# Optimization experiments

Measured on AMD Instinct MI355X. Metric: run time of the kernel, lower is better.

Reference implementation:

```python
import jax, jax.numpy as jnp
import numpy as np

N = 50000      # nodes
E = 200000     # edges
F_IN = 128     # input features
H = 1024       # hidden
C = 16         # classes
K = 3          # TAGConv hops
EPS = 1e-5


def setup_inputs() -> dict:
    key = jax.random.key(0)
    ks = jax.random.split(key, 12)
    s = 0.02
    x = jax.random.normal(ks[0], (N, F_IN), jnp.float32)
    edge_index = jax.random.randint(ks[1], (2, E), 0, N, dtype=jnp.int64)
    weight = jax.random.uniform(ks[2], (E,), jnp.float32)
    return {
        "x": x,
        "edge_index": edge_index,
        "weight": weight,
        "W1": jax.random.normal(ks[3], (K + 1, F_IN, H), jnp.float32) * s,
        "b1": jnp.zeros((H,), jnp.float32),
        "g1": jnp.ones((H,), jnp.float32),
        "be1": jnp.zeros((H,), jnp.float32),
        "a1": jnp.ones((H,), jnp.float32),
        "W2": jax.random.normal(ks[4], (K + 1, H, H), jnp.float32) * s,
        "b2": jnp.zeros((H,), jnp.float32),
        "g2": jnp.ones((H,), jnp.float32),
        "be2": jnp.zeros((H,), jnp.float32),
        "a2": jnp.ones((H,), jnp.float32),
        "W3": jax.random.normal(ks[5], (K + 1, H, C), jnp.float32) * s,
        "b3": jnp.zeros((C,), jnp.float32),
    }


def _edge_norm(weight, src, dst):
    # gcn_norm without self-loops: deg from edge weights at target nodes
    deg = jax.ops.segment_sum(weight, dst, num_segments=N)
    safe = jnp.where(deg > 0, deg, 1.0)
    dinv = jnp.where(deg > 0, jax.lax.rsqrt(safe), 0.0)
    norm_w = dinv[src] * weight * dinv[dst]
    cnt = jax.ops.segment_sum(jnp.ones((E,), weight.dtype), dst, num_segments=N)
    cnt_inv = jnp.where(cnt > 0, 1.0 / jnp.where(cnt > 0, cnt, 1.0), 0.0)
    return norm_w, cnt_inv


def _tagconv(x, W, b, src, dst, norm_w, cnt_inv):
    # out = sum_k lin_k(x_k), x_k = mean-aggr of norm_w * x_{k-1}[src] at dst
    out = x @ W[0]
    h = x
    for k in range(1, K + 1):
        msg = norm_w[:, None] * h[src]                       # [E, d]
        h = jax.ops.segment_sum(msg, dst, num_segments=N) * cnt_inv[:, None]
        out = out + h @ W[k]
    return out + b


def _graphnorm(x, g, be, a):
    # single graph: per-graph stats = global stats over nodes
    mean = jnp.mean(x, axis=0)
    out = x - a * mean
    var = jnp.mean(out * out, axis=0)
    return g * out / jnp.sqrt(var + EPS) + be


def reference(x, edge_index, weight, W1, b1, g1, be1, a1,
              W2, b2, g2, be2, a2, W3, b3):
    src, dst = edge_index[0], edge_index[1]
    norm_w, cnt_inv = _edge_norm(weight, src, dst)
    h = jax.nn.elu(_tagconv(x, W1, b1, src, dst, norm_w, cnt_inv))
    h = _graphnorm(h, g1, be1, a1)
    h = jax.nn.elu(_tagconv(h, W2, b2, src, dst, norm_w, cnt_inv))
    h = _graphnorm(h, g2, be2, a2)
    return _tagconv(h, W3, b3, src, dst, norm_w, cnt_inv)
```

## Files before the change

### kernel.cpp

```cpp
#include <hip/hip_runtime.h>
#include <hip/hip_bf16.h>
#include <math.h>

#define N_NODES 50000
#define N_EDGES 200000
#define FIN 128
#define HID 1024
#define NCLS 16
#define EPSN 1e-5f
#define NPAD 50048
#define MT 391
#define EPITCH 136

typedef __attribute__((ext_vector_type(8))) short short8;
typedef __attribute__((ext_vector_type(8))) unsigned short ushort8;
typedef __attribute__((ext_vector_type(4))) unsigned short u16x4;
typedef __attribute__((ext_vector_type(4))) float f32x4;

static __device__ __forceinline__ float bf2f(unsigned short u) {
  union { unsigned int i; float f; } v; v.i = ((unsigned int)u) << 16; return v.f;
}
static __device__ __forceinline__ unsigned short f2bf(float f) {
  __hip_bfloat16 h = __float2bfloat16(f);
  return *(unsigned short*)&h;
}

#define ASYNC16(gsrc, ldst)                                                   \
  __builtin_amdgcn_global_load_lds(                                           \
      (const __attribute__((address_space(1))) void*)(gsrc),                  \
      (__attribute__((address_space(3))) void*)(ldst), 16, 0, 0)


__global__ __launch_bounds__(256) void k_deg_cnt(const int* __restrict__ dst,
                                                 const float* __restrict__ w,
                                                 float* deg, int* cnt) {
  int e = blockIdx.x * 256 + threadIdx.x;
  if (e < N_EDGES) {
    int d = dst[e];
    atomicAdd(&deg[d], w[e]);
    atomicAdd(&cnt[d], 1);
  }
}

__global__ __launch_bounds__(256) void k_normw(const int* __restrict__ src,
                                               const int* __restrict__ dst,
                                               const float* __restrict__ w,
                                               const float* __restrict__ deg,
                                               float* __restrict__ normw) {
  int e = blockIdx.x * 256 + threadIdx.x;
  if (e < N_EDGES) {
    float ds = deg[src[e]], dd = deg[dst[e]];
    float a = ds > 0.f ? rsqrtf(ds) : 0.f;
    float b = dd > 0.f ? rsqrtf(dd) : 0.f;
    normw[e] = a * w[e] * b;
  }
}

__global__ __launch_bounds__(256) void k_cntinv(const int* __restrict__ cnt,
                                                float* __restrict__ cnt_inv) {
  int n = blockIdx.x * 256 + threadIdx.x;
  if (n < N_NODES) {
    int c = cnt[n];
    cnt_inv[n] = c > 0 ? 1.f / (float)c : 0.f;
  }
}

__global__ __launch_bounds__(1024) void k_scan_a(const int* __restrict__ cnt,
                                                 int* __restrict__ rowptr,
                                                 int* __restrict__ bsums) {
  __shared__ int sm[1024];
  int tid = threadIdx.x;
  int i = blockIdx.x * 1024 + tid;
  int v = (i < N_NODES) ? cnt[i] : 0;
  sm[tid] = v;
  __syncthreads();
  for (int off = 1; off < 1024; off <<= 1) {
    int t = (tid >= off) ? sm[tid - off] : 0;
    __syncthreads();
    sm[tid] += t;
    __syncthreads();
  }
  if (i < N_NODES) rowptr[i] = sm[tid] - v;
  if (tid == 1023) bsums[blockIdx.x] = sm[1023];
}

__global__ void k_scan_b(int* bsums, int nb) {
  if (threadIdx.x == 0 && blockIdx.x == 0) {
    int s = 0;
    for (int i = 0; i < nb; ++i) { int t = bsums[i]; bsums[i] = s; s += t; }
  }
}

__global__ __launch_bounds__(1024) void k_scan_c(int* __restrict__ rowptr,
                                                 const int* __restrict__ bsums) {
  int i = blockIdx.x * 1024 + threadIdx.x;
  if (i < N_NODES) rowptr[i] += bsums[blockIdx.x];
}

__global__ __launch_bounds__(256) void k_fill(const int* __restrict__ src,
                                              const int* __restrict__ dst,
                                              const float* __restrict__ normw,
                                              const int* __restrict__ rowptr,
                                              int* __restrict__ fill,
                                              int2* __restrict__ csr_ew) {
  int e = blockIdx.x * 256 + threadIdx.x;
  if (e < N_EDGES) {
    int d = dst[e];
    int pos = rowptr[d] + atomicAdd(&fill[d], 1);
    csr_ew[pos] = make_int2(src[e], __float_as_int(normw[e]));
  }
}


__global__ void k_transpose_bf16(const float* __restrict__ in,
                                 __hip_bfloat16* __restrict__ out, int K, int N) {
  __shared__ float tile[32][33];
  int kb = blockIdx.x * 32, nb = blockIdx.y * 32;
  int tx = threadIdx.x, ty = threadIdx.y;
  for (int i = ty; i < 32; i += 8) tile[i][tx] = in[(size_t)(kb + i) * N + nb + tx];
  __syncthreads();
  for (int i = ty; i < 32; i += 8)
    out[(size_t)(nb + i) * K + kb + tx] = __float2bfloat16(tile[tx][i]);
}

__global__ void k_transpose_scale_bf16(const float* __restrict__ in,
                                       __hip_bfloat16* __restrict__ out, int K, int N,
                                       const float* __restrict__ alpha) {
  __shared__ float tile[32][33];
  int kb = blockIdx.x * 32, nb = blockIdx.y * 32;
  int tx = threadIdx.x, ty = threadIdx.y;
  for (int i = ty; i < 32; i += 8) tile[i][tx] = in[(size_t)(kb + i) * N + nb + tx];
  __syncthreads();
  float sc = alpha[(kb + tx) & (HID - 1)];
  for (int i = ty; i < 32; i += 8)
    out[(size_t)(nb + i) * K + kb + tx] = __float2bfloat16(tile[tx][i] * sc);
}

__global__ __launch_bounds__(256) void k_ck_part(const float* __restrict__ W2,
                                                 const float* __restrict__ beta,
                                                 const float* __restrict__ b2,
                                                 float* __restrict__ ck) {
  int k3 = blockIdx.x;
  int ch = blockIdx.y;
  int tid = threadIdx.x;
  float acc[4] = {0.f, 0.f, 0.f, 0.f};
  const float* Wk = W2 + (size_t)k3 * HID * HID;
  int i0 = ch * 64;
  for (int in = i0; in < i0 + 64; ++in) {
    float s = beta[in];
    const float* row = Wk + (size_t)in * HID;
#pragma unroll
    for (int j = 0; j < 4; ++j) acc[j] += s * row[tid + j * 256];
  }
#pragma unroll
  for (int j = 0; j < 4; ++j) {
    float v = acc[j];
    if (k3 == 0 && ch == 0) v += b2[tid + j * 256];
    atomicAdd(&ck[k3 * HID + tid + j * 256], v);
  }
}

__global__ __launch_bounds__(64) void k_ck3(const float* __restrict__ W3,
                                            const float* __restrict__ beta,
                                            float* __restrict__ ck3) {
  int t = threadIdx.x;
  int k = t >> 4, j = t & 15;
  float acc = 0.f;
  for (int in = 0; in < HID; ++in)
    acc += beta[in] * W3[((size_t)k * HID + in) * 16 + j];
  ck3[t] = acc;
}

__global__ __launch_bounds__(256) void k_packw3(const float* __restrict__ W3,
                                                __hip_bfloat16* __restrict__ W3T,
                                                const float* __restrict__ alpha) {
  int idx = blockIdx.x * 256 + threadIdx.x;
  if (idx < 4 * 1024 * 16) {
    int k3 = idx >> 14, r = idx & 16383, k = r >> 4, j = r & 15;
    W3T[(size_t)(k3 * 16 + j) * 1024 + k] = __float2bfloat16(W3[idx] * alpha[k]);
  }
}

__global__ __launch_bounds__(256) void k_x_to_bf16(const float* __restrict__ x,
                                                   unsigned short* __restrict__ xc) {
  int i = blockIdx.x * 256 + threadIdx.x;
  if (i < N_NODES * FIN / 4) {
    int n = i >> 5, c4 = i & 31;
    const float4 v = ((const float4*)x)[i];
    u16x4 o;
    o[0] = f2bf(v.x); o[1] = f2bf(v.y); o[2] = f2bf(v.z); o[3] = f2bf(v.w);
    *(u16x4*)&xc[(size_t)n * 512 + c4 * 4] = o;
  }
}


template <int W>
__global__ __launch_bounds__(256) void k_spmm_v(
    const unsigned short* __restrict__ src_t, int sp,
    unsigned short* __restrict__ dst_t, int dp,
    const int* __restrict__ rowptr, const int* __restrict__ cnt,
    const float* __restrict__ cnt_inv,
    const int2* __restrict__ csr_ew) {
  constexpr int G = W / 8;
  int gl = blockIdx.x * 256 + threadIdx.x;
  int node = gl / G;
  if (node >= N_NODES) return;
  int fl = (gl % G) * 8;
  int beg = rowptr[node], end = beg + cnt[node];
  float acc[8] = {0.f, 0.f, 0.f, 0.f, 0.f, 0.f, 0.f, 0.f};
  int i = beg;
  for (; i + 1 < end; i += 2) {
    int2 e0 = csr_ew[i], e1 = csr_ew[i + 1];
    float w0 = __int_as_float(e0.y), w1 = __int_as_float(e1.y);
    ushort8 v0 = *(const ushort8*)&src_t[(size_t)e0.x * sp + fl];
    ushort8 v1 = *(const ushort8*)&src_t[(size_t)e1.x * sp + fl];
#pragma unroll
    for (int j = 0; j < 8; ++j) acc[j] += w0 * bf2f(v0[j]) + w1 * bf2f(v1[j]);
  }
  if (i < end) {
    int2 e0 = csr_ew[i];
    float w0 = __int_as_float(e0.y);
    ushort8 v0 = *(const ushort8*)&src_t[(size_t)e0.x * sp + fl];
#pragma unroll
    for (int j = 0; j < 8; ++j) acc[j] += w0 * bf2f(v0[j]);
  }
  float ci = cnt_inv[node];
  ushort8 o;
#pragma unroll
  for (int j = 0; j < 8; ++j) o[j] = f2bf(acc[j] * ci);
  *(ushort8*)&dst_t[(size_t)node * dp + fl] = o;
}

__global__ __launch_bounds__(256) void k_spmm16(const float* __restrict__ src_t, int sp,
                                                const float* __restrict__ addend, int ap,
                                                const float* __restrict__ b3,
                                                float* __restrict__ out, int op,
                                                const int* __restrict__ rowptr,
                                                const int* __restrict__ cnt,
                                                const float* __restrict__ cnt_inv,
                                                const int2* __restrict__ csr_ew) {
  int idx = blockIdx.x * 256 + threadIdx.x;
  if (idx >= N_NODES * 16) return;
  int node = idx >> 4, f = idx & 15;
  int beg = rowptr[node], ne = cnt[node];
  float acc = 0.f;
  for (int i = 0; i < ne; ++i) {
    int2 e = csr_ew[beg + i];
    acc += __int_as_float(e.y) * src_t[(size_t)e.x * sp + f];
  }
  float r = acc * cnt_inv[node] + addend[(size_t)node * ap + f];
  if (b3) r += b3[f];
  out[(size_t)node * op + f] = r;
}


__global__ __launch_bounds__(256, 4) void k_gemm(
    const unsigned short* __restrict__ A, int lda,
    const unsigned short* __restrict__ BT, int ldb,
    const unsigned short* __restrict__ Cinit, int ldci,
    void* __restrict__ Cout, int ldc, int cbf16,
    int M, int Nout, int K,
    const float* __restrict__ bias, int do_elu) {
  __shared__ __align__(16) unsigned short smem[128 * EPITCH];
  int tid = threadIdx.x;
  int wave = tid >> 6, lane = tid & 63;
  int wm = wave >> 1, wn = wave & 1;
  int l15 = lane & 15, quad = lane >> 4;
  int im = blockIdx.y, in_ = blockIdx.x;

  f32x4 acc[4][4];
  if (Cinit) {
    {
      int r = tid >> 1, hf = tid & 1;
      const unsigned short* gsrc =
          &Cinit[(size_t)(im * 128 + r) * ldci + in_ * 128 + hf * 64];
#pragma unroll
      for (int v = 0; v < 8; ++v)
        *(ushort8*)&smem[r * EPITCH + hf * 64 + v * 8] = *(const ushort8*)&gsrc[v * 8];
    }
    __syncthreads();
#pragma unroll
    for (int i = 0; i < 4; ++i)
#pragma unroll
      for (int j = 0; j < 4; ++j)
#pragma unroll
        for (int reg = 0; reg < 4; ++reg)
          acc[i][j][reg] =
              bf2f(smem[(wm * 64 + i * 16 + quad * 4 + reg) * EPITCH + wn * 64 + j * 16 + l15]);
    __syncthreads();
  } else {
#pragma unroll
    for (int i = 0; i < 4; ++i)
#pragma unroll
      for (int j = 0; j < 4; ++j) acc[i][j] = (f32x4){0.f, 0.f, 0.f, 0.f};
  }

  int srow = tid >> 2;
  int sl = (tid & 3) ^ (srow & 3) ^ ((srow >> 2) & 3);
  const unsigned short* gA0 = &A[(size_t)(im * 128 + srow) * lda + sl * 8];
  const unsigned short* gA1 = &A[(size_t)(im * 128 + 64 + srow) * lda + sl * 8];
  const unsigned short* gB0 = &BT[(size_t)(in_ * 128 + srow) * ldb + sl * 8];
  const unsigned short* gB1 = &BT[(size_t)(in_ * 128 + 64 + srow) * ldb + sl * 8];
  unsigned short* ldsA = smem;
  unsigned short* ldsB = smem + 8192;
  int woff0 = (wave * 64) * 8;
  int woff1 = (256 + wave * 64) * 8;
  int rsl = (quad ^ (l15 & 3) ^ (l15 >> 2)) * 8;

  auto stage = [&](int k0, int p) {
    ASYNC16(gA0 + k0, &ldsA[p * 4096 + woff0]);
    ASYNC16(gA1 + k0, &ldsA[p * 4096 + woff1]);
    ASYNC16(gB0 + k0, &ldsB[p * 4096 + woff0]);
    ASYNC16(gB1 + k0, &ldsB[p * 4096 + woff1]);
  };
  auto compute = [&](int p) {
    short8 af[4], bf[4];
#pragma unroll
    for (int i = 0; i < 4; ++i)
      af[i] = *(const short8*)&ldsA[p * 4096 + (wm * 64 + i * 16 + l15) * 32 + rsl];
#pragma unroll
    for (int j = 0; j < 4; ++j)
      bf[j] = *(const short8*)&ldsB[p * 4096 + (wn * 64 + j * 16 + l15) * 32 + rsl];
#pragma unroll
    for (int i = 0; i < 4; ++i)
#pragma unroll
      for (int j = 0; j < 4; ++j)
        acc[i][j] = __builtin_amdgcn_mfma_f32_16x16x32_bf16(af[i], bf[j], acc[i][j], 0, 0, 0);
  };

  stage(0, 0);
  __syncthreads();
  int p = 0;
  for (int k0 = 32; k0 < K; k0 += 32) {
    stage(k0, p ^ 1);
    compute(p);
    __syncthreads();
    p ^= 1;
  }
  compute(p);
  __syncthreads();

  if (cbf16) {
#pragma unroll
    for (int i = 0; i < 4; ++i)
#pragma unroll
      for (int j = 0; j < 4; ++j) {
        int cg = in_ * 128 + wn * 64 + j * 16 + l15;
        float bv = bias ? bias[cg] : 0.f;
#pragma unroll
        for (int reg = 0; reg < 4; ++reg) {
          float v = acc[i][j][reg] + bv;
          if (do_elu) v = v > 0.f ? v : expm1f(v);
          smem[(wm * 64 + i * 16 + quad * 4 + reg) * EPITCH + wn * 64 + j * 16 + l15] = f2bf(v);
        }
      }
    __syncthreads();
    int r = tid >> 1, hf = tid & 1;
    unsigned short* gdst =
        (unsigned short*)Cout + (size_t)(im * 128 + r) * ldc + in_ * 128 + hf * 64;
#pragma unroll
    for (int v = 0; v < 8; ++v)
      *(ushort8*)&gdst[v * 8] = *(const ushort8*)&smem[r * EPITCH + hf * 64 + v * 8];
  } else {
#pragma unroll
    for (int i = 0; i < 4; ++i) {
      int r0 = im * 128 + wm * 64 + i * 16 + quad * 4;
#pragma unroll
      for (int j = 0; j < 4; ++j) {
        int c = in_ * 128 + wn * 64 + j * 16 + l15;
        if (c < Nout) {
#pragma unroll
          for (int reg = 0; reg < 4; ++reg) {
            int r = r0 + reg;
            if (r < M) {
              float v = acc[i][j][reg];
              if (bias) v += bias[c];
              if (do_elu) v = v > 0.f ? v : expm1f(v);
              ((float*)Cout)[(size_t)r * ldc + c] = v;
            }
          }
        }
      }
    }
  }
}


__global__ __launch_bounds__(512) void k_colstats(const unsigned short* __restrict__ h,
                                                  float* __restrict__ stats) {
  __shared__ float sm[4 * 2048];
  int tid = threadIdx.x;
  int f0 = (tid & 127) * 8;
  int q = tid >> 7;
  int r0 = blockIdx.y * 128 + q * 32;
  int r1 = r0 + 32; if (r1 > N_NODES) r1 = N_NODES;
  float s[8] = {0,0,0,0,0,0,0,0}, s2[8] = {0,0,0,0,0,0,0,0};
  for (int r = r0; r < r1; ++r) {
    ushort8 v = *(const ushort8*)&h[(size_t)r * HID + f0];
#pragma unroll
    for (int j = 0; j < 8; ++j) { float x = bf2f(v[j]); s[j] += x; s2[j] += x * x; }
  }
#pragma unroll
  for (int j = 0; j < 8; ++j) {
    sm[q * 2048 + f0 + j] = s[j];
    sm[q * 2048 + 1024 + f0 + j] = s2[j];
  }
  __syncthreads();
  for (int idx = tid; idx < 2048; idx += 512) {
    float v = sm[idx] + sm[2048 + idx] + sm[4096 + idx] + sm[6144 + idx];
    atomicAdd(&stats[idx], v);
  }
}

__global__ __launch_bounds__(256) void k_finalize(const float* __restrict__ g,
                                                  const float* __restrict__ be,
                                                  const float* __restrict__ a,
                                                  float* __restrict__ stats) {
  int f = blockIdx.x * 256 + threadIdx.x;
  if (f < HID) {
    float m = stats[f] / (float)N_NODES;
    float ex2 = stats[HID + f] / (float)N_NODES;
    float av = a[f];
    float var = ex2 - 2.f * av * m * m + av * av * m * m;
    float alpha = g[f] * rsqrtf(var + EPSN);
    stats[2 * HID + f] = alpha;
    stats[3 * HID + f] = be[f] - alpha * av * m;
  }
}


extern "C" void kernel_launch(void* const* d_in, const int* in_sizes, int n_in,
                              void* d_out, int out_size, void* d_ws, size_t ws_size,
                              hipStream_t stream) {
  const float* x   = (const float*)d_in[0];
  const int*   ei  = (const int*)d_in[1];
  const float* w   = (const float*)d_in[2];
  const float* W1  = (const float*)d_in[3];
  const float* b1  = (const float*)d_in[4];
  const float* g1  = (const float*)d_in[5];
  const float* be1 = (const float*)d_in[6];
  const float* a1  = (const float*)d_in[7];
  const float* W2  = (const float*)d_in[8];
  const float* b2  = (const float*)d_in[9];
  const float* g2  = (const float*)d_in[10];
  const float* be2 = (const float*)d_in[11];
  const float* a2  = (const float*)d_in[12];
  const float* W3  = (const float*)d_in[13];
  const float* b3  = (const float*)d_in[14];
  float* out = (float*)d_out;

  const int* srcI = ei;
  const int* dstI = ei + N_EDGES;

  char* base = (char*)d_ws;
  size_t off = 0;
  auto alloc = [&](size_t bytes) -> char* {
    char* p = base + off;
    off += (bytes + 255) & ~(size_t)255;
    return p;
  };

  float* deg      = (float*)alloc(N_NODES * 4);
  int*   cnt      = (int*)alloc(N_NODES * 4);
  float* cnt_inv  = (float*)alloc(N_NODES * 4);
  float* normw    = (float*)alloc(N_EDGES * 4);
  int*   rowptr   = (int*)alloc((N_NODES + 1) * 4);
  int*   fill     = (int*)alloc(N_NODES * 4);
  int*   bsums    = (int*)alloc(64 * 4);
  int2*  csr_ew   = (int2*)alloc((size_t)N_EDGES * 8);
  float* stats    = (float*)alloc(4 * HID * 4);
  float* ck       = (float*)alloc(4 * HID * 4);
  float* ck3      = (float*)alloc(64 * 4);
  __hip_bfloat16* W1T = (__hip_bfloat16*)alloc((size_t)1024 * 512 * 2);
  __hip_bfloat16* W2T = (__hip_bfloat16*)alloc((size_t)1024 * 4096 * 2);
  __hip_bfloat16* W3T = (__hip_bfloat16*)alloc((size_t)128 * 1024 * 2);
  const size_t FT = (size_t)NPAD * HID * 2;
  unsigned short* T0 = (unsigned short*)alloc(FT);
  unsigned short* T1 = (unsigned short*)alloc(FT);
  size_t rem = (ws_size > off) ? (ws_size - off) : 0;
  bool full = rem >= FT + 1024;
  unsigned short *T2 = nullptr, *Q = nullptr, *R = nullptr;
  int wcols = 0;
  if (full) {
    T2 = (unsigned short*)alloc(FT);
  } else {
    wcols = 512;
    if (rem < 2 * (size_t)NPAD * 512 * 2 + 1024) wcols = 256;
    if (wcols == 256 && rem < 2 * (size_t)NPAD * 256 * 2 + 1024) wcols = 128;
    Q = (unsigned short*)alloc((size_t)NPAD * wcols * 2);
    R = (unsigned short*)alloc((size_t)NPAD * wcols * 2);
  }
  float* Z  = (float*)T0;
  float* t0 = (float*)((char*)T0 + (size_t)16 * 1024 * 1024);
  float* t1 = (float*)((char*)T0 + (size_t)24 * 1024 * 1024);
  (void)n_in; (void)in_sizes; (void)out_size;

  const int EB = (N_EDGES + 255) / 256;
  const int NB = (N_NODES + 255) / 256;

  (void)hipMemsetAsync(deg, 0, N_NODES * 4, stream);
  (void)hipMemsetAsync(cnt, 0, N_NODES * 4, stream);
  (void)hipMemsetAsync(fill, 0, N_NODES * 4, stream);
  k_deg_cnt<<<EB, 256, 0, stream>>>(dstI, w, deg, cnt);
  k_normw<<<EB, 256, 0, stream>>>(srcI, dstI, w, deg, normw);
  k_cntinv<<<NB, 256, 0, stream>>>(cnt, cnt_inv);
  k_scan_a<<<49, 1024, 0, stream>>>(cnt, rowptr, bsums);
  k_scan_b<<<1, 64, 0, stream>>>(bsums, 49);
  k_scan_c<<<49, 1024, 0, stream>>>(rowptr, bsums);
  k_fill<<<EB, 256, 0, stream>>>(srcI, dstI, normw, rowptr, fill, csr_ew);

  k_transpose_bf16<<<dim3(512 / 32, 1024 / 32), dim3(32, 8), 0, stream>>>(W1, W1T, 512, 1024);

  const unsigned short* W2Tu = (const unsigned short*)W2T;

  k_x_to_bf16<<<(N_NODES * FIN / 4 + 255) / 256, 256, 0, stream>>>(x, T1);
  {
    int blocks = (N_NODES * 16 + 255) / 256;
    for (int k = 1; k <= 3; ++k)
      k_spmm_v<128><<<blocks, 256, 0, stream>>>(
          T1 + (k - 1) * FIN, 512, T1 + k * FIN, 512,
          rowptr, cnt, cnt_inv, csr_ew);
  }
  k_gemm<<<dim3(8, MT), 256, 0, stream>>>(
      T1, 512, (const unsigned short*)W1T, 512,
      nullptr, 0, T0, HID, 1, N_NODES, HID, 512, b1, 1);
  (void)hipMemsetAsync(stats, 0, 2 * HID * 4, stream);
  k_colstats<<<dim3(1, MT), 512, 0, stream>>>(T0, stats);
  k_finalize<<<4, 256, 0, stream>>>(g1, be1, a1, stats);
  k_transpose_scale_bf16<<<dim3(4096 / 32, 1024 / 32), dim3(32, 8), 0, stream>>>(
      W2, W2T, 4096, 1024, stats + 2 * HID);
  (void)hipMemsetAsync(ck, 0, 4 * HID * 4, stream);
  k_ck_part<<<dim3(4, 16), 256, 0, stream>>>(W2, stats + 3 * HID, b2, ck);

  if (full) {
    const int SPB = (N_NODES * 128 + 255) / 256;
    k_gemm<<<dim3(8, MT), 256, 0, stream>>>(
        T0, 1024, W2Tu + 3 * 1024, 4096,
        nullptr, 0, T1, 1024, 1, N_NODES, 1024, 1024, ck + 3 * 1024, 0);
    k_spmm_v<1024><<<SPB, 256, 0, stream>>>(T1, 1024, T2, 1024,
                                            rowptr, cnt, cnt_inv, csr_ew);
    k_gemm<<<dim3(8, MT), 256, 0, stream>>>(
        T0, 1024, W2Tu + 2 * 1024, 4096,
        T2, 1024, T1, 1024, 1, N_NODES, 1024, 1024, ck + 2 * 1024, 0);
    k_spmm_v<1024><<<SPB, 256, 0, stream>>>(T1, 1024, T2, 1024,
                                            rowptr, cnt, cnt_inv, csr_ew);
    k_gemm<<<dim3(8, MT), 256, 0, stream>>>(
        T0, 1024, W2Tu + 1 * 1024, 4096,
        T2, 1024, T1, 1024, 1, N_NODES, 1024, 1024, ck + 1 * 1024, 0);
    k_spmm_v<1024><<<SPB, 256, 0, stream>>>(T1, 1024, T2, 1024,
                                            rowptr, cnt, cnt_inv, csr_ew);
    k_gemm<<<dim3(8, MT), 256, 0, stream>>>(
        T0, 1024, W2Tu + 0 * 1024, 4096,
        T2, 1024, T1, 1024, 1, N_NODES, 1024, 1024, ck + 0 * 1024, 1);
  } else {
    auto spmm_w = [&](const unsigned short* s, unsigned short* d) {
      int blocks = (N_NODES * (wcols / 8) + 255) / 256;
      if (wcols == 512)
        k_spmm_v<512><<<blocks, 256, 0, stream>>>(s, wcols, d, wcols,
            rowptr, cnt, cnt_inv, csr_ew);
      else if (wcols == 256)
        k_spmm_v<256><<<blocks, 256, 0, stream>>>(s, wcols, d, wcols,
            rowptr, cnt, cnt_inv, csr_ew);
      else
        k_spmm_v<128><<<blocks, 256, 0, stream>>>(s, wcols, d, wcols,
            rowptr, cnt, cnt_inv, csr_ew);
    };
    for (int c = 0; c < HID; c += wcols) {
      const unsigned short* Wb = W2Tu + (size_t)c * 4096;
      k_gemm<<<dim3(wcols / 128, MT), 256, 0, stream>>>(
          T0, 1024, Wb + 3 * 1024, 4096,
          nullptr, 0, Q, wcols, 1, N_NODES, wcols, 1024, ck + 3 * 1024 + c, 0);
      spmm_w(Q, R);
      k_gemm<<<dim3(wcols / 128, MT), 256, 0, stream>>>(
          T0, 1024, Wb + 2 * 1024, 4096,
          R, wcols, Q, wcols, 1, N_NODES, wcols, 1024, ck + 2 * 1024 + c, 0);
      spmm_w(Q, R);
      k_gemm<<<dim3(wcols / 128, MT), 256, 0, stream>>>(
          T0, 1024, Wb + 1 * 1024, 4096,
          R, wcols, Q, wcols, 1, N_NODES, wcols, 1024, ck + 1 * 1024 + c, 0);
      spmm_w(Q, R);
      k_gemm<<<dim3(wcols / 128, MT), 256, 0, stream>>>(
          T0, 1024, Wb + 0 * 1024, 4096,
          R, wcols, T1 + c, 1024, 1, N_NODES, wcols, 1024, ck + 0 * 1024 + c, 1);
    }
  }
  (void)hipMemsetAsync(stats, 0, 2 * HID * 4, stream);
  k_colstats<<<dim3(1, MT), 512, 0, stream>>>(T1, stats);
  k_finalize<<<4, 256, 0, stream>>>(g2, be2, a2, stats);
  k_packw3<<<(65536 + 255) / 256, 256, 0, stream>>>(W3, W3T, stats + 2 * HID);
  k_ck3<<<1, 64, 0, stream>>>(W3, stats + 3 * HID, ck3);

  k_gemm<<<dim3(1, MT), 256, 0, stream>>>(
      T1, 1024, (const unsigned short*)W3T, 1024,
      nullptr, 0, Z, 64, 0, N_NODES, 64, 1024, ck3, 0);
  const int SB = (N_NODES * 16 + 255) / 256;
  k_spmm16<<<SB, 256, 0, stream>>>(Z + 48, 64, Z + 32, 64, nullptr, t0, 16,
                                   rowptr, cnt, cnt_inv, csr_ew);
  k_spmm16<<<SB, 256, 0, stream>>>(t0, 16, Z + 16, 64, nullptr, t1, 16,
                                   rowptr, cnt, cnt_inv, csr_ew);
  k_spmm16<<<SB, 256, 0, stream>>>(t1, 16, Z + 0, 64, b3, out, 16,
                                   rowptr, cnt, cnt_inv, csr_ew);
}
```

Baseline: 1.835 ms.

## Fuse column statistics into GEMM epilogue, fold cnt_inv into edge weights, widen SpMM

Removes the separate column-statistics pass by accumulating per-column sum and sum-of-squares of the bf16 outputs inside the GEMM epilogue, reduced through shared memory and added with atomics. This avoids re-reading the full 50000x1024 activation twice. It also pre-multiplies the mean-aggregation factor cnt_inv into the CSR edge weights and merges the normw and cnt_inv kernels. The 1024-wide SpMM now handles 16 features per thread instead of 8. The costs are extra epilogue work and atomics in the GEMM, and fewer threads in the wide SpMM.

```diff
diff --git a/kernel.cpp b/kernel.cpp
--- a/kernel.cpp
+++ b/kernel.cpp
@@ -42,11 +42,13 @@
   }
 }
 
-__global__ __launch_bounds__(256) void k_normw(const int* __restrict__ src,
-                                               const int* __restrict__ dst,
-                                               const float* __restrict__ w,
-                                               const float* __restrict__ deg,
-                                               float* __restrict__ normw) {
+__global__ __launch_bounds__(256) void k_normw_cntinv(const int* __restrict__ src,
+                                                      const int* __restrict__ dst,
+                                                      const float* __restrict__ w,
+                                                      const float* __restrict__ deg,
+                                                      const int* __restrict__ cnt,
+                                                      float* __restrict__ normw,
+                                                      float* __restrict__ cnt_inv) {
   int e = blockIdx.x * 256 + threadIdx.x;
   if (e < N_EDGES) {
     float ds = deg[src[e]], dd = deg[dst[e]];
@@ -54,14 +56,9 @@
     float b = dd > 0.f ? rsqrtf(dd) : 0.f;
     normw[e] = a * w[e] * b;
   }
-}
-
-__global__ __launch_bounds__(256) void k_cntinv(const int* __restrict__ cnt,
-                                                float* __restrict__ cnt_inv) {
-  int n = blockIdx.x * 256 + threadIdx.x;
-  if (n < N_NODES) {
-    int c = cnt[n];
-    cnt_inv[n] = c > 0 ? 1.f / (float)c : 0.f;
+  if (e < N_NODES) {
+    int c = cnt[e];
+    cnt_inv[e] = c > 0 ? 1.f / (float)c : 0.f;
   }
 }
 
@@ -100,6 +97,7 @@
 __global__ __launch_bounds__(256) void k_fill(const int* __restrict__ src,
                                               const int* __restrict__ dst,
                                               const float* __restrict__ normw,
+                                              const float* __restrict__ cnt_inv,
                                               const int* __restrict__ rowptr,
                                               int* __restrict__ fill,
                                               int2* __restrict__ csr_ew) {
@@ -107,7 +105,7 @@
   if (e < N_EDGES) {
     int d = dst[e];
     int pos = rowptr[d] + atomicAdd(&fill[d], 1);
-    csr_ew[pos] = make_int2(src[e], __float_as_int(normw[e]));
+    csr_ew[pos] = make_int2(src[e], __float_as_int(normw[e] * cnt_inv[d]));
   }
 }
 
@@ -194,41 +192,55 @@
 }
 
 
-template <int W>
+template <int W, int FPL>
 __global__ __launch_bounds__(256) void k_spmm_v(
     const unsigned short* __restrict__ src_t, int sp,
     unsigned short* __restrict__ dst_t, int dp,
     const int* __restrict__ rowptr, const int* __restrict__ cnt,
-    const float* __restrict__ cnt_inv,
     const int2* __restrict__ csr_ew) {
-  constexpr int G = W / 8;
+  constexpr int G = W / FPL;
+  constexpr int NV = FPL / 8;
   int gl = blockIdx.x * 256 + threadIdx.x;
   int node = gl / G;
   if (node >= N_NODES) return;
-  int fl = (gl % G) * 8;
+  int fl = (gl % G) * FPL;
   int beg = rowptr[node], end = beg + cnt[node];
-  float acc[8] = {0.f, 0.f, 0.f, 0.f, 0.f, 0.f, 0.f, 0.f};
+  float acc[FPL];
+#pragma unroll
+  for (int j = 0; j < FPL; ++j) acc[j] = 0.f;
   int i = beg;
   for (; i + 1 < end; i += 2) {
     int2 e0 = csr_ew[i], e1 = csr_ew[i + 1];
     float w0 = __int_as_float(e0.y), w1 = __int_as_float(e1.y);
-    ushort8 v0 = *(const ushort8*)&src_t[(size_t)e0.x * sp + fl];
-    ushort8 v1 = *(const ushort8*)&src_t[(size_t)e1.x * sp + fl];
-#pragma unroll
-    for (int j = 0; j < 8; ++j) acc[j] += w0 * bf2f(v0[j]) + w1 * bf2f(v1[j]);
+    ushort8 v0[NV], v1[NV];
+#pragma unroll
+    for (int h = 0; h < NV; ++h) {
+      v0[h] = *(const ushort8*)&src_t[(size_t)e0.x * sp + fl + h * 8];
+      v1[h] = *(const ushort8*)&src_t[(size_t)e1.x * sp + fl + h * 8];
+    }
+#pragma unroll
+    for (int h = 0; h < NV; ++h)
+#pragma unroll
+      for (int j = 0; j < 8; ++j)
+        acc[h * 8 + j] += w0 * bf2f(v0[h][j]) + w1 * bf2f(v1[h][j]);
   }
   if (i < end) {
     int2 e0 = csr_ew[i];
     float w0 = __int_as_float(e0.y);
-    ushort8 v0 = *(const ushort8*)&src_t[(size_t)e0.x * sp + fl];
-#pragma unroll
-    for (int j = 0; j < 8; ++j) acc[j] += w0 * bf2f(v0[j]);
-  }
-  float ci = cnt_inv[node];
-  ushort8 o;
-#pragma unroll
-  for (int j = 0; j < 8; ++j) o[j] = f2bf(acc[j] * ci);
-  *(ushort8*)&dst_t[(size_t)node * dp + fl] = o;
+#pragma unroll
+    for (int h = 0; h < NV; ++h) {
+      ushort8 v0 = *(const ushort8*)&src_t[(size_t)e0.x * sp + fl + h * 8];
+#pragma unroll
+      for (int j = 0; j < 8; ++j) acc[h * 8 + j] += w0 * bf2f(v0[j]);
+    }
+  }
+#pragma unroll
+  for (int h = 0; h < NV; ++h) {
+    ushort8 o;
+#pragma unroll
+    for (int j = 0; j < 8; ++j) o[j] = f2bf(acc[h * 8 + j]);
+    *(ushort8*)&dst_t[(size_t)node * dp + fl + h * 8] = o;
+  }
 }
 
 __global__ __launch_bounds__(256) void k_spmm16(const float* __restrict__ src_t, int sp,
@@ -237,7 +249,6 @@
                                                 float* __restrict__ out, int op,
                                                 const int* __restrict__ rowptr,
                                                 const int* __restrict__ cnt,
-                                                const float* __restrict__ cnt_inv,
                                                 const int2* __restrict__ csr_ew) {
   int idx = blockIdx.x * 256 + threadIdx.x;
   if (idx >= N_NODES * 16) return;
@@ -248,7 +259,7 @@
     int2 e = csr_ew[beg + i];
     acc += __int_as_float(e.y) * src_t[(size_t)e.x * sp + f];
   }
-  float r = acc * cnt_inv[node] + addend[(size_t)node * ap + f];
+  float r = acc + addend[(size_t)node * ap + f];
   if (b3) r += b3[f];
   out[(size_t)node * op + f] = r;
 }
@@ -260,7 +271,8 @@
     const unsigned short* __restrict__ Cinit, int ldci,
     void* __restrict__ Cout, int ldc, int cbf16,
     int M, int Nout, int K,
-    const float* __restrict__ bias, int do_elu) {
+    const float* __restrict__ bias, int do_elu,
+    float* __restrict__ stats_out, int stats_off) {
   __shared__ __align__(16) unsigned short smem[128 * EPITCH];
   int tid = threadIdx.x;
   int wave = tid >> 6, lane = tid & 63;
@@ -341,6 +353,7 @@
   __syncthreads();
 
   if (cbf16) {
+    float sl0[4] = {0.f, 0.f, 0.f, 0.f}, sl2[4] = {0.f, 0.f, 0.f, 0.f};
 #pragma unroll
     for (int i = 0; i < 4; ++i)
 #pragma unroll
@@ -351,16 +364,48 @@
         for (int reg = 0; reg < 4; ++reg) {
           float v = acc[i][j][reg] + bv;
           if (do_elu) v = v > 0.f ? v : expm1f(v);
-          smem[(wm * 64 + i * 16 + quad * 4 + reg) * EPITCH + wn * 64 + j * 16 + l15] = f2bf(v);
+          unsigned short b = f2bf(v);
+          smem[(wm * 64 + i * 16 + quad * 4 + reg) * EPITCH + wn * 64 + j * 16 + l15] = b;
+          if (stats_out) {
+            int r = im * 128 + wm * 64 + i * 16 + quad * 4 + reg;
+            if (r < M) {
+              float vq = bf2f(b);
+              sl0[j] += vq; sl2[j] += vq * vq;
+            }
+          }
         }
       }
     __syncthreads();
-    int r = tid >> 1, hf = tid & 1;
-    unsigned short* gdst =
-        (unsigned short*)Cout + (size_t)(im * 128 + r) * ldc + in_ * 128 + hf * 64;
-#pragma unroll
-    for (int v = 0; v < 8; ++v)
-      *(ushort8*)&gdst[v * 8] = *(const ushort8*)&smem[r * EPITCH + hf * 64 + v * 8];
+    {
+      int r = tid >> 1, hf = tid & 1;
+      unsigned short* gdst =
+          (unsigned short*)Cout + (size_t)(im * 128 + r) * ldc + in_ * 128 + hf * 64;
+#pragma unroll
+      for (int v = 0; v < 8; ++v)
+        *(ushort8*)&gdst[v * 8] = *(const ushort8*)&smem[r * EPITCH + hf * 64 + v * 8];
+    }
+    if (stats_out) {
+      __syncthreads();
+      float* fs = (float*)smem;
+      int slot = wm * 4 + quad;
+#pragma unroll
+      for (int j = 0; j < 4; ++j) {
+        int c = wn * 64 + j * 16 + l15;
+        fs[slot * 128 + c] = sl0[j];
+        fs[1024 + slot * 128 + c] = sl2[j];
+      }
+      __syncthreads();
+      if (tid < 128) {
+        float a0 = 0.f, a1 = 0.f;
+#pragma unroll
+        for (int s = 0; s < 8; ++s) {
+          a0 += fs[s * 128 + tid];
+          a1 += fs[1024 + s * 128 + tid];
+        }
+        atomicAdd(&stats_out[stats_off + in_ * 128 + tid], a0);
+        atomicAdd(&stats_out[HID + stats_off + in_ * 128 + tid], a1);
+      }
+    }
   } else {
 #pragma unroll
     for (int i = 0; i < 4; ++i) {
@@ -385,32 +430,6 @@
   }
 }
 
-
-__global__ __launch_bounds__(512) void k_colstats(const unsigned short* __restrict__ h,
-                                                  float* __restrict__ stats) {
-  __shared__ float sm[4 * 2048];
-  int tid = threadIdx.x;
-  int f0 = (tid & 127) * 8;
-  int q = tid >> 7;
-  int r0 = blockIdx.y * 128 + q * 32;
-  int r1 = r0 + 32; if (r1 > N_NODES) r1 = N_NODES;
-  float s[8] = {0,0,0,0,0,0,0,0}, s2[8] = {0,0,0,0,0,0,0,0};
-  for (int r = r0; r < r1; ++r) {
-    ushort8 v = *(const ushort8*)&h[(size_t)r * HID + f0];
-#pragma unroll
-    for (int j = 0; j < 8; ++j) { float x = bf2f(v[j]); s[j] += x; s2[j] += x * x; }
-  }
-#pragma unroll
-  for (int j = 0; j < 8; ++j) {
-    sm[q * 2048 + f0 + j] = s[j];
-    sm[q * 2048 + 1024 + f0 + j] = s2[j];
-  }
-  __syncthreads();
-  for (int idx = tid; idx < 2048; idx += 512) {
-    float v = sm[idx] + sm[2048 + idx] + sm[4096 + idx] + sm[6144 + idx];
-    atomicAdd(&stats[idx], v);
-  }
-}
 
 __global__ __launch_bounds__(256) void k_finalize(const float* __restrict__ g,
                                                   const float* __restrict__ be,
@@ -496,18 +515,16 @@
   (void)n_in; (void)in_sizes; (void)out_size;
 
   const int EB = (N_EDGES + 255) / 256;
-  const int NB = (N_NODES + 255) / 256;
 
   (void)hipMemsetAsync(deg, 0, N_NODES * 4, stream);
   (void)hipMemsetAsync(cnt, 0, N_NODES * 4, stream);
   (void)hipMemsetAsync(fill, 0, N_NODES * 4, stream);
   k_deg_cnt<<<EB, 256, 0, stream>>>(dstI, w, deg, cnt);
-  k_normw<<<EB, 256, 0, stream>>>(srcI, dstI, w, deg, normw);
-  k_cntinv<<<NB, 256, 0, stream>>>(cnt, cnt_inv);
+  k_normw_cntinv<<<EB, 256, 0, stream>>>(srcI, dstI, w, deg, cnt, normw, cnt_inv);
   k_scan_a<<<49, 1024, 0, stream>>>(cnt, rowptr, bsums);
   k_scan_b<<<1, 64, 0, stream>>>(bsums, 49);
   k_scan_c<<<49, 1024, 0, stream>>>(rowptr, bsums);
-  k_fill<<<EB, 256, 0, stream>>>(srcI, dstI, normw, rowptr, fill, csr_ew);
+  k_fill<<<EB, 256, 0, stream>>>(srcI, dstI, normw, cnt_inv, rowptr, fill, csr_ew);
 
   k_transpose_bf16<<<dim3(512 / 32, 1024 / 32), dim3(32, 8), 0, stream>>>(W1, W1T, 512, 1024);
 
@@ -517,15 +534,14 @@
   {
     int blocks = (N_NODES * 16 + 255) / 256;
     for (int k = 1; k <= 3; ++k)
-      k_spmm_v<128><<<blocks, 256, 0, stream>>>(
+      k_spmm_v<128, 8><<<blocks, 256, 0, stream>>>(
           T1 + (k - 1) * FIN, 512, T1 + k * FIN, 512,
-          rowptr, cnt, cnt_inv, csr_ew);
-  }
+          rowptr, cnt, csr_ew);
+  }
+  (void)hipMemsetAsync(stats, 0, 2 * HID * 4, stream);
   k_gemm<<<dim3(8, MT), 256, 0, stream>>>(
       T1, 512, (const unsigned short*)W1T, 512,
-      nullptr, 0, T0, HID, 1, N_NODES, HID, 512, b1, 1);
-  (void)hipMemsetAsync(stats, 0, 2 * HID * 4, stream);
-  k_colstats<<<dim3(1, MT), 512, 0, stream>>>(T0, stats);
+      nullptr, 0, T0, HID, 1, N_NODES, HID, 512, b1, 1, stats, 0);
   k_finalize<<<4, 256, 0, stream>>>(g1, be1, a1, stats);
   k_transpose_scale_bf16<<<dim3(4096 / 32, 1024 / 32), dim3(32, 8), 0, stream>>>(
       W2, W2T, 4096, 1024, stats + 2 * HID);
@@ -533,71 +549,71 @@
   k_ck_part<<<dim3(4, 16), 256, 0, stream>>>(W2, stats + 3 * HID, b2, ck);
 
   if (full) {
-    const int SPB = (N_NODES * 128 + 255) / 256;
+    const int SPB = (N_NODES * 64 + 255) / 256;
     k_gemm<<<dim3(8, MT), 256, 0, stream>>>(
         T0, 1024, W2Tu + 3 * 1024, 4096,
-        nullptr, 0, T1, 1024, 1, N_NODES, 1024, 1024, ck + 3 * 1024, 0);
-    k_spmm_v<1024><<<SPB, 256, 0, stream>>>(T1, 1024, T2, 1024,
-                                            rowptr, cnt, cnt_inv, csr_ew);
+        nullptr, 0, T1, 1024, 1, N_NODES, 1024, 1024, ck + 3 * 1024, 0, nullptr, 0);
+    k_spmm_v<1024, 16><<<SPB, 256, 0, stream>>>(T1, 1024, T2, 1024,
+                                                rowptr, cnt, csr_ew);
     k_gemm<<<dim3(8, MT), 256, 0, stream>>>(
         T0, 1024, W2Tu + 2 * 1024, 4096,
-        T2, 1024, T1, 1024, 1, N_NODES, 1024, 1024, ck + 2 * 1024, 0);
-    k_spmm_v<1024><<<SPB, 256, 0, stream>>>(T1, 1024, T2, 1024,
-                                            rowptr, cnt, cnt_inv, csr_ew);
+        T2, 1024, T1, 1024, 1, N_NODES, 1024, 1024, ck + 2 * 1024, 0, nullptr, 0);
+    k_spmm_v<1024, 16><<<SPB, 256, 0, stream>>>(T1, 1024, T2, 1024,
+                                                rowptr, cnt, csr_ew);
     k_gemm<<<dim3(8, MT), 256, 0, stream>>>(
         T0, 1024, W2Tu + 1 * 1024, 4096,
-        T2, 1024, T1, 1024, 1, N_NODES, 1024, 1024, ck + 1 * 1024, 0);
-    k_spmm_v<1024><<<SPB, 256, 0, stream>>>(T1, 1024, T2, 1024,
-                                            rowptr, cnt, cnt_inv, csr_ew);
+        T2, 1024, T1, 1024, 1, N_NODES, 1024, 1024, ck + 1 * 1024, 0, nullptr, 0);
+    k_spmm_v<1024, 16><<<SPB, 256, 0, stream>>>(T1, 1024, T2, 1024,
+                                                rowptr, cnt, csr_ew);
+    (void)hipMemsetAsync(stats, 0, 2 * HID * 4, stream);
     k_gemm<<<dim3(8, MT), 256, 0, stream>>>(
         T0, 1024, W2Tu + 0 * 1024, 4096,
-        T2, 1024, T1, 1024, 1, N_NODES, 1024, 1024, ck + 0 * 1024, 1);
+        T2, 1024, T1, 1024, 1, N_NODES, 1024, 1024, ck + 0 * 1024, 1, stats, 0);
   } else {
     auto spmm_w = [&](const unsigned short* s, unsigned short* d) {
       int blocks = (N_NODES * (wcols / 8) + 255) / 256;
       if (wcols == 512)
-        k_spmm_v<512><<<blocks, 256, 0, stream>>>(s, wcols, d, wcols,
-            rowptr, cnt, cnt_inv, csr_ew);
+        k_spmm_v<512, 8><<<blocks, 256, 0, stream>>>(s, wcols, d, wcols,
+            rowptr, cnt, csr_ew);
       else if (wcols == 256)
-        k_spmm_v<256><<<blocks, 256, 0, stream>>>(s, wcols, d, wcols,
-            rowptr, cnt, cnt_inv, csr_ew);
+        k_spmm_v<256, 8><<<blocks, 256, 0, stream>>>(s, wcols, d, wcols,
+            rowptr, cnt, csr_ew);
       else
-        k_spmm_v<128><<<blocks, 256, 0, stream>>>(s, wcols, d, wcols,
-            rowptr, cnt, cnt_inv, csr_ew);
+        k_spmm_v<128, 8><<<blocks, 256, 0, stream>>>(s, wcols, d, wcols,
+            rowptr, cnt, csr_ew);
     };
+    (void)hipMemsetAsync(stats, 0, 2 * HID * 4, stream);
     for (int c = 0; c < HID; c += wcols) {
       const unsigned short* Wb = W2Tu + (size_t)c * 4096;
       k_gemm<<<dim3(wcols / 128, MT), 256, 0, stream>>>(
           T0, 1024, Wb + 3 * 1024, 4096,
-          nullptr, 0, Q, wcols, 1, N_NODES, wcols, 1024, ck + 3 * 1024 + c, 0);
+          nullptr, 0, Q, wcols, 1, N_NODES, wcols, 1024, ck + 3 * 1024 + c, 0, nullptr, 0);
       spmm_w(Q, R);
       k_gemm<<<dim3(wcols / 128, MT), 256, 0, stream>>>(
           T0, 1024, Wb + 2 * 1024, 4096,
-          R, wcols, Q, wcols, 1, N_NODES, wcols, 1024, ck + 2 * 1024 + c, 0);
+          R, wcols, Q, wcols, 1, N_NODES, wcols, 1024, ck + 2 * 1024 + c, 0, nullptr, 0);
       spmm_w(Q, R);
       k_gemm<<<dim3(wcols / 128, MT), 256, 0, stream>>>(
           T0, 1024, Wb + 1 * 1024, 4096,
-          R, wcols, Q, wcols, 1, N_NODES, wcols, 1024, ck + 1 * 1024 + c, 0);
+          R, wcols, Q, wcols, 1, N_NODES, wcols, 1024, ck + 1 * 1024 + c, 0, nullptr, 0);
       spmm_w(Q, R);
       k_gemm<<<dim3(wcols / 128, MT), 256, 0, stream>>>(
           T0, 1024, Wb + 0 * 1024, 4096,
-          R, wcols, T1 + c, 1024, 1, N_NODES, wcols, 1024, ck + 0 * 1024 + c, 1);
+          R, wcols, T1 + c, 1024, 1, N_NODES, wcols, 1024, ck + 0 * 1024 + c, 1, stats, c);
     }
   }
-  (void)hipMemsetAsync(stats, 0, 2 * HID * 4, stream);
-  k_colstats<<<dim3(1, MT), 512, 0, stream>>>(T1, stats);
   k_finalize<<<4, 256, 0, stream>>>(g2, be2, a2, stats);
   k_packw3<<<(65536 + 255) / 256, 256, 0, stream>>>(W3, W3T, stats + 2 * HID);
   k_ck3<<<1, 64, 0, stream>>>(W3, stats + 3 * HID, ck3);
 
   k_gemm<<<dim3(1, MT), 256, 0, stream>>>(
       T1, 1024, (const unsigned short*)W3T, 1024,
-      nullptr, 0, Z, 64, 0, N_NODES, 64, 1024, ck3, 0);
+      nullptr, 0, Z, 64, 0, N_NODES, 64, 1024, ck3, 0, nullptr, 0);
   const int SB = (N_NODES * 16 + 255) / 256;
   k_spmm16<<<SB, 256, 0, stream>>>(Z + 48, 64, Z + 32, 64, nullptr, t0, 16,
-                                   rowptr, cnt, cnt_inv, csr_ew);
+                                   rowptr, cnt, csr_ew);
   k_spmm16<<<SB, 256, 0, stream>>>(t0, 16, Z + 16, 64, nullptr, t1, 16,
-                                   rowptr, cnt, cnt_inv, csr_ew);
+                                   rowptr, cnt, csr_ew);
   k_spmm16<<<SB, 256, 0, stream>>>(t1, 16, Z + 0, 64, b3, out, 16,
-                                   rowptr, cnt, cnt_inv, csr_ew);
-}
+                                   rowptr, cnt, csr_ew);
+}
```

New measurement: 1.860 ms. About the same (+1.4%).
